# Kernel optimization log

Measured on AMD Instinct MI355X. Metric: run time of the kernel, lower is better.

Reference implementation:

```python
import jax, jax.numpy as jnp
import numpy as np

N_Q_HEADS = 16
N_KV_HEADS = 4
HEAD_DIM = 128
SLIDING_WINDOW = 1024
ROPE_BASE = 1024


def _rope_tables(L, dim):
    # half-truncate RoPE: first dim//4 freqs geometric, next dim//4 zero
    freqs = (1.0 / ROPE_BASE) ** jnp.linspace(0.0, 1.0, num=dim // 4)
    freqs = jnp.concatenate([freqs, jnp.zeros(dim // 4, dtype=freqs.dtype)])
    theta = jnp.arange(L, dtype=jnp.float32)[:, None] * freqs[None, :]  # (L, dim/2)
    cos = jnp.cos(theta)[None, :, None, :]  # (1, L, 1, dim/2)
    sin = jnp.sin(theta)[None, :, None, :]
    return cos, sin


def _rotate(x, cos, sin):
    # x: (B, L, H, D)
    x1, x2 = jnp.split(x, 2, axis=-1)
    return jnp.concatenate([x1 * cos + x2 * sin, -x1 * sin + x2 * cos], axis=-1)


def setup_inputs() -> dict:
    key = jax.random.key(0)
    k1, k2, k3, k4 = jax.random.split(key, 4)
    B, L, D = 1, 2048, 2048
    qkv_dim = (N_Q_HEADS + 2 * N_KV_HEADS) * HEAD_DIM  # 3072
    return {
        "x": jax.random.normal(k1, (B, L, D), dtype=jnp.float32),
        "Wqkv": jax.random.normal(k2, (D, qkv_dim), dtype=jnp.float32) * (D ** -0.5),
        "Wo": jax.random.normal(k3, (N_Q_HEADS * HEAD_DIM, D), dtype=jnp.float32) * ((N_Q_HEADS * HEAD_DIM) ** -0.5),
        "s": jax.random.normal(k4, (1, N_Q_HEADS), dtype=jnp.float32) * 0.1,
    }


def reference(x, Wqkv, Wo, s):
    B, L, D = x.shape
    H, QM, hd = N_KV_HEADS, N_Q_HEADS // N_KV_HEADS, HEAD_DIM

    proj = x @ Wqkv  # (B, L, (Hq + 2*Hkv) * hd)
    q, k, v = jnp.split(proj, (N_Q_HEADS * hd, (N_Q_HEADS + N_KV_HEADS) * hd), axis=-1)

    cos, sin = _rope_tables(L, hd)
    q = _rotate(q.reshape(B, L, -1, hd), cos, sin).reshape(B, L, H, QM, hd)
    k = _rotate(k.reshape(B, L, H, hd), cos, sin)
    v = v.reshape(B, L, H, hd)

    sm_scale = 1.0 / jnp.sqrt(jnp.float32(hd))
    q_pos = jnp.arange(L)[None, :, None]
    k_pos = jnp.arange(L)[None, None, :]
    causal = q_pos >= k_pos                       # (1, L, L)
    window = q_pos < k_pos + SLIDING_WINDOW       # index % 2 == 0 -> window active
    mask = causal & window

    # (B, H, M, Lq, Lk) attention logits
    attn = jnp.einsum("bqhmd,bkhd->bhmqk", q, k) * sm_scale
    # NOTE: faithful to source: -inf placed WHERE mask is True
    attn = jnp.where(mask, -jnp.inf, attn)

    sink = jnp.broadcast_to(s.reshape(B, H, QM, 1, 1), (B, H, QM, L, 1))
    w = jax.nn.softmax(jnp.concatenate([attn, sink], axis=-1), axis=-1)[..., :-1]

    out = jnp.einsum("bhmqk,bkhd->bqhmd", w, v).reshape(B, L, -1)
    return out @ Wo
```

## Files before the change

### kernel.cpp

```cpp
#include <hip/hip_runtime.h>
#include <hip/hip_bf16.h>
#include <math.h>

typedef __bf16 bf16;
typedef __bf16 bf16x8 __attribute__((ext_vector_type(8)));
typedef __bf16 bf16x4v __attribute__((ext_vector_type(4)));
typedef short s16x4 __attribute__((ext_vector_type(4)));
typedef float f32x4 __attribute__((ext_vector_type(4)));

#define GLD16(gp, lp) __builtin_amdgcn_global_load_lds( \
    (__attribute__((address_space(1))) void*)(void*)(gp), \
    (__attribute__((address_space(3))) void*)(lp), 16, 0, 0)

#define L_SEQ 2048
#define D_MODEL 2048
#define QKV_N 3072
#define HD 128
#define QSCALE 0.1275310242959836f
#define LOG2E 1.4426950408889634f

__global__ __launch_bounds__(256) void prep(const float* __restrict__ x,
                                            const float* __restrict__ Wqkv,
                                            const float* __restrict__ Wo,
                                            bf16* __restrict__ xb,
                                            bf16* __restrict__ wqkvT,
                                            bf16* __restrict__ woT) {
    __shared__ float tile[32][33];
    int bid = blockIdx.x;
    if (bid < 4096) {
        int idx = (bid * 256 + threadIdx.x) * 4;
        float4 f = *(const float4*)(x + idx);
        bf16x4v o;
        o.x = (bf16)f.x; o.y = (bf16)f.y; o.z = (bf16)f.z; o.w = (bf16)f.w;
        *(bf16x4v*)(xb + idx) = o;
        return;
    }
    bid -= 4096;
    const float* src; bf16* dst; long ld_s, ld_d; int bx, by;
    if (bid < 6144) { bx = bid % 96; by = bid / 96; src = Wqkv; dst = wqkvT; ld_s = QKV_N; ld_d = D_MODEL; }
    else { bid -= 6144; bx = bid & 63; by = bid >> 6; src = Wo; dst = woT; ld_s = D_MODEL; ld_d = D_MODEL; }
    const int tx = threadIdx.x & 31, ty = threadIdx.x >> 5;
    const long c = bx * 32 + tx, r0 = by * 32;
#pragma unroll
    for (int i = 0; i < 4; ++i)
        tile[ty + i * 8][tx] = src[(r0 + ty + i * 8) * ld_s + c];
    __syncthreads();
    const long c0 = bx * 32;
#pragma unroll
    for (int i = 0; i < 4; ++i)
        dst[(c0 + ty + i * 8) * ld_d + r0 + tx] = (bf16)tile[tx][ty + i * 8];
}

#define GEMM64_BODY(KDIM)                                                        \
    __shared__ __align__(16) bf16 As[64 * 32];                                   \
    __shared__ __align__(16) bf16 Bs[128 * 32];                                  \
    const int tid = threadIdx.x;                                                 \
    const int wid = tid >> 6, lane = tid & 63;                                   \
    const int quad = lane >> 4, l15 = lane & 15;                                 \
    const long m0 = (long)blockIdx.y * 64, n0 = (long)blockIdx.x * 128;          \
    const int srowA = wid * 16 + (lane >> 2);                                    \
    const int srowB = wid * 32 + (lane >> 2);                                    \
    const int scol = ((lane & 3) ^ ((lane >> 3) & 3)) * 8;                       \
    f32x4 acc[8];                                                                \
    _Pragma("unroll")                                                            \
    for (int j = 0; j < 8; ++j) acc[j] = (f32x4){0.f, 0.f, 0.f, 0.f};            \
    const bf16* Ap  = A  + (m0 + srowA) * KDIM + scol;                           \
    const bf16* Bp  = Bt + (n0 + srowB) * KDIM + scol;                           \
    const bf16* Bp2 = Bp + (long)16 * KDIM;                                      \
    bf16* lA  = &As[(wid * 16) * 32];                                            \
    bf16* lB  = &Bs[(wid * 32) * 32];                                            \
    bf16* lB2 = &Bs[(wid * 32 + 16) * 32];                                       \
    const int rsw = ((l15 >> 1) & 3);                                            \
    for (int k0 = 0; k0 < KDIM; k0 += 32) {                                      \
        GLD16(Ap + k0, lA);                                                      \
        GLD16(Bp + k0, lB);                                                      \
        GLD16(Bp2 + k0, lB2);                                                    \
        __syncthreads();                                                         \
        bf16x8 af = *(const bf16x8*)&As[(wid * 16 + l15) * 32 + (quad ^ rsw) * 8]; \
        bf16x8 bfr[8];                                                           \
        _Pragma("unroll")                                                        \
        for (int j = 0; j < 8; ++j)                                              \
            bfr[j] = *(const bf16x8*)&Bs[(j * 16 + l15) * 32 + (quad ^ rsw) * 8]; \
        _Pragma("unroll")                                                        \
        for (int j = 0; j < 8; ++j)                                              \
            acc[j] = __builtin_amdgcn_mfma_f32_16x16x32_bf16(af, bfr[j], acc[j], 0, 0, 0); \
        __syncthreads();                                                         \
    }

__global__ __launch_bounds__(256) void gemm_qkv(const bf16* __restrict__ A,
                                                const bf16* __restrict__ Bt,
                                                bf16* __restrict__ Qb,
                                                bf16* __restrict__ Kb,
                                                bf16* __restrict__ Vtb) {
    const int head = blockIdx.x;
    GEMM64_BODY(D_MODEL)

    if (head < 20) {
        const float sc = head < 16 ? QSCALE : 1.0f;
        bf16* dst = head < 16 ? Qb + (long)head * L_SEQ * HD
                              : Kb + (long)(head - 16) * L_SEQ * HD;
#pragma unroll
        for (int jj = 0; jj < 2; ++jj) {
            const int d0 = jj * 16 + l15;
            const float freq = exp2f((float)d0 * (-10.0f / 31.0f));
#pragma unroll
            for (int r = 0; r < 4; ++r) {
                const long row = m0 + wid * 16 + quad * 4 + r;
                float sn, cs;
                sincosf((float)row * freq, &sn, &cs);
                const float x1 = acc[jj][r], x2 = acc[jj + 4][r];
                dst[row * HD + d0]      = (bf16)((x1 * cs + x2 * sn) * sc);
                dst[row * HD + d0 + 64] = (bf16)((x2 * cs - x1 * sn) * sc);
            }
        }
#pragma unroll
        for (int jj = 2; jj < 4; ++jj) {
            const int d0 = jj * 16 + l15;
#pragma unroll
            for (int r = 0; r < 4; ++r) {
                const long row = m0 + wid * 16 + quad * 4 + r;
                dst[row * HD + d0]      = (bf16)(acc[jj][r] * sc);
                dst[row * HD + d0 + 64] = (bf16)(acc[jj + 4][r] * sc);
            }
        }
    } else {
        bf16* dst = Vtb + (long)(head - 20) * HD * L_SEQ;
        const long m = m0 + wid * 16 + quad * 4;
#pragma unroll
        for (int j = 0; j < 8; ++j) {
            const int d = j * 16 + l15;
            bf16x4v vv;
#pragma unroll
            for (int r = 0; r < 4; ++r) vv[r] = (bf16)acc[j][r];
            *(bf16x4v*)(dst + (long)d * L_SEQ + m) = vv;
        }
    }
}

__global__ __launch_bounds__(256) void gemm_out(const bf16* __restrict__ A,
                                                const bf16* __restrict__ Bt,
                                                float* __restrict__ C) {
    GEMM64_BODY(D_MODEL)
#pragma unroll
    for (int j = 0; j < 8; ++j) {
        const long m = m0 + wid * 16 + quad * 4;
        const long n = n0 + j * 16 + l15;
#pragma unroll
        for (int r = 0; r < 4; ++r)
            C[(m + r) * (long)D_MODEL + n] = acc[j][r];
    }
}

__global__ __launch_bounds__(512, 2) void attn_kernel(const bf16* __restrict__ Qb,
                                                      const bf16* __restrict__ Kb,
                                                      const bf16* __restrict__ Vtb,
                                                      const float* __restrict__ sink,
                                                      bf16* __restrict__ Ob) {
    __shared__ __align__(1024) char smem[131072];

    const int bid = blockIdx.x;
    const int t  = bid & 15;
    const int hq = bid >> 4;
    const int h = hq >> 2;
    const int q0 = t * 128;
    const int tid = threadIdx.x;
    const int wid8 = tid >> 6;
    const int g = wid8 >> 2;
    const int w = wid8 & 3;
    const int lane = tid & 63;
    const int quad = lane >> 4, l15 = lane & 15;

    const bf16* Qg = Qb + (long)hq * L_SEQ * HD;
    const bf16* Kg = Kb + (long)h * L_SEQ * HD;
    const bf16* Vg = Vtb + (long)h * HD * L_SEQ;

    bf16x8 qb[2][4];
#pragma unroll
    for (int rf = 0; rf < 2; ++rf)
#pragma unroll
        for (int kkd = 0; kkd < 4; ++kkd)
            qb[rf][kkd] = *(const bf16x8*)(Qg + (long)(q0 + w * 32 + rf * 16 + l15) * HD
                                              + kkd * 32 + quad * 8);

    f32x4 oaccT[2][8];
#pragma unroll
    for (int rf = 0; rf < 2; ++rf)
#pragma unroll
        for (int j = 0; j < 8; ++j) oaccT[rf][j] = (f32x4){0.f, 0.f, 0.f, 0.f};
    float lacc[2] = {0.f, 0.f};

    const int locnt = (2 * t - 14 > 0) ? (2 * t - 14) : 0;
    const int n = locnt + 32 - 2 * t;
    const int iters = (n + 1) >> 1;

    auto stage = [&](int it2, int buf) {
        const int i = 2 * it2 + g;
        if (i >= n) return;
        const int kt = (i < locnt) ? i : (2 * t + (i - locnt));
        const int k0 = kt * 64;
        bf16* Ksb  = (bf16*)(smem + g * 65536 + buf * 32768);
        bf16* Vtsb = (bf16*)(smem + g * 65536 + buf * 32768 + 16384);
#pragma unroll
        for (int ii = 0; ii < 4; ++ii) {
            int rowb = w * 16 + ii * 4;
            int row = rowb + quad;
            GLD16(Kg + (long)(k0 + row) * HD + ((l15 ^ (row & 7)) * 8), &Ksb[rowb * 128]);
        }
#pragma unroll
        for (int ii = 0; ii < 4; ++ii) {
            int rowb = w * 32 + ii * 8;
            int row = rowb + (lane >> 3);
            GLD16(Vg + (long)row * L_SEQ + k0 + (((lane & 7) ^ (row & 7)) * 8), &Vtsb[rowb * 64]);
        }
    };

    stage(0, 0);

    for (int it = 0; it < iters; ++it) {
        __syncthreads();
        if (it + 1 < iters) stage(it + 1, (it + 1) & 1);

        const int i = 2 * it + g;
        if (i >= n) continue;
        const int kt = (i < locnt) ? i : (2 * t + (i - locnt));
        const int k0 = kt * 64;
        const bf16* Ks  = (const bf16*)(smem + g * 65536 + (it & 1) * 32768);
        const bf16* Vts = (const bf16*)(smem + g * 65536 + (it & 1) * 32768 + 16384);

        f32x4 sacc[2][4];
#pragma unroll
        for (int kb = 0; kb < 4; ++kb) {
            bf16x8 ka[4];
#pragma unroll
            for (int kkd = 0; kkd < 4; ++kkd)
                ka[kkd] = *(const bf16x8*)&Ks[(kb * 16 + l15) * 128 +
                                              (((kkd * 4 + quad) ^ (l15 & 7)) * 8)];
#pragma unroll
            for (int rf = 0; rf < 2; ++rf) {
                f32x4 acc = (f32x4){0.f, 0.f, 0.f, 0.f};
#pragma unroll
                for (int kkd = 0; kkd < 4; ++kkd)
                    acc = __builtin_amdgcn_mfma_f32_16x16x32_bf16(ka[kkd], qb[rf][kkd], acc, 0, 0, 0);
                sacc[rf][kb] = acc;
            }
        }

        const bool bnd = (kt == 2 * t) || (kt == 2 * t + 1) ||
                         (kt == 2 * t - 15) || (kt == 2 * t - 16);
        s16x4 pb[2][4];
#pragma unroll
        for (int rf = 0; rf < 2; ++rf) {
            const int qq = q0 + w * 32 + rf * 16 + l15;
#pragma unroll
            for (int kb = 0; kb < 4; ++kb) {
#pragma unroll
                for (int r = 0; r < 4; ++r) {
                    float v = sacc[rf][kb][r];
                    if (bnd) {
                        const int kk = k0 + kb * 16 + quad * 4 + r;
                        if (!((kk > qq) || (kk <= qq - 1024))) v = -1e30f;
                    }
                    const float p = exp2f(v);
                    lacc[rf] += p;
                    bf16 hp = (bf16)p;
                    pb[rf][kb][r] = __builtin_bit_cast(short, hp);
                }
            }
        }

#pragma unroll
        for (int j = 0; j < 8; ++j) {
            const int drow = j * 16 + l15;
#pragma unroll
            for (int kq = 0; kq < 4; ++kq) {
                const int pc = ((kq * 2 + (quad >> 1)) ^ (l15 & 7));
                s16x4 va = *(const s16x4*)((const char*)&Vts[drow * 64] + pc * 16 + (quad & 1) * 8);
#pragma unroll
                for (int rf = 0; rf < 2; ++rf)
                    oaccT[rf][j] = __builtin_amdgcn_mfma_f32_16x16x16bf16_1k(
                        va, pb[rf][kq], oaccT[rf][j], 0, 0, 0);
            }
        }
    }

#pragma unroll
    for (int rf = 0; rf < 2; ++rf) {
        lacc[rf] += __shfl_xor(lacc[rf], 16, 64);
        lacc[rf] += __shfl_xor(lacc[rf], 32, 64);
    }

    __syncthreads();
    float* Obuf = (float*)smem;
    float* lbuf = (float*)(smem + 67584);
    if (g == 1) {
#pragma unroll
        for (int rf = 0; rf < 2; ++rf) {
            const int ql = w * 32 + rf * 16 + l15;
#pragma unroll
            for (int j = 0; j < 8; ++j)
                *(f32x4*)&Obuf[ql * 132 + j * 16 + quad * 4] = oaccT[rf][j];
            if (quad == 0) lbuf[ql] = lacc[rf];
        }
    }
    __syncthreads();
    if (g == 0) {
        const float sv2 = sink[hq] * LOG2E;
#pragma unroll
        for (int rf = 0; rf < 2; ++rf) {
            const int ql = w * 32 + rf * 16 + l15;
            const float ltot = lacc[rf] + lbuf[ql] + exp2f(sv2);
            const float inv = 1.0f / ltot;
            bf16* dst = Ob + (long)(q0 + ql) * D_MODEL + hq * HD;
#pragma unroll
            for (int j = 0; j < 8; ++j) {
                f32x4 o2 = *(const f32x4*)&Obuf[ql * 132 + j * 16 + quad * 4];
                bf16x4v ov;
#pragma unroll
                for (int r = 0; r < 4; ++r)
                    ov[r] = (bf16)((oaccT[rf][j][r] + o2[r]) * inv);
                *(bf16x4v*)(dst + j * 16 + quad * 4) = ov;
            }
        }
    }
}

extern "C" void kernel_launch(void* const* d_in, const int* in_sizes, int n_in,
                              void* d_out, int out_size, void* d_ws, size_t ws_size,
                              hipStream_t stream) {
    (void)in_sizes; (void)n_in; (void)out_size; (void)ws_size;
    const float* x    = (const float*)d_in[0];
    const float* Wqkv = (const float*)d_in[1];
    const float* Wo   = (const float*)d_in[2];
    const float* s    = (const float*)d_in[3];
    float* out = (float*)d_out;

    char* ws = (char*)d_ws;
    bf16* xb    = (bf16*)ws;  ws += (size_t)D_MODEL * D_MODEL * 2;
    bf16* wqkvT = (bf16*)ws;  ws += (size_t)QKV_N * D_MODEL * 2;
    bf16* woT   = (bf16*)ws;  ws += (size_t)D_MODEL * D_MODEL * 2;
    bf16* Qb    = (bf16*)ws;  ws += (size_t)16 * L_SEQ * HD * 2;
    bf16* Kb    = (bf16*)ws;  ws += (size_t)4 * L_SEQ * HD * 2;
    bf16* Vtb   = (bf16*)ws;  ws += (size_t)4 * HD * L_SEQ * 2;
    bf16* attnb = (bf16*)ws;  ws += (size_t)L_SEQ * D_MODEL * 2;

    prep<<<14336, 256, 0, stream>>>(x, Wqkv, Wo, xb, wqkvT, woT);

    gemm_qkv<<<dim3(QKV_N / 128, L_SEQ / 64), 256, 0, stream>>>(
        xb, wqkvT, Qb, Kb, Vtb);

    attn_kernel<<<256, 512, 0, stream>>>(Qb, Kb, Vtb, s, attnb);

    gemm_out<<<dim3(D_MODEL / 128, L_SEQ / 64), 256, 0, stream>>>(
        attnb, woT, out);
}
```

Before: 232.3 us.

## Split attention key range across separate blocks with a combine kernel

Each 512-thread attention block, whose two wave groups split the key tiles and merged through shared memory, becomes two independent 256-thread blocks. Each new block owns half the key tiles and writes unnormalized bf16 partial outputs and row sums to workspace. A new combine kernel adds the two partials, adds the sink term, normalizes and writes the attention output. The aim is finer-grained scheduling and smaller blocks with less shared memory each. In exchange it adds an extra kernel launch, global traffic for the partials, and bf16 rounding of the partials before they are summed. The workspace is reorganized so the partials reuse the region of the converted input, which is dead after the QKV GEMM.

```diff
diff --git a/kernel.cpp b/kernel.cpp
--- a/kernel.cpp
+++ b/kernel.cpp
@@ -151,22 +151,21 @@
     }
 }
 
-__global__ __launch_bounds__(512, 2) void attn_kernel(const bf16* __restrict__ Qb,
-                                                      const bf16* __restrict__ Kb,
-                                                      const bf16* __restrict__ Vtb,
-                                                      const float* __restrict__ sink,
-                                                      bf16* __restrict__ Ob) {
-    __shared__ __align__(1024) char smem[131072];
+__global__ __launch_bounds__(256, 2) void attn_p(const bf16* __restrict__ Qb,
+                                                 const bf16* __restrict__ Kb,
+                                                 const bf16* __restrict__ Vtb,
+                                                 bf16* __restrict__ Opart,
+                                                 float* __restrict__ lpart) {
+    __shared__ __align__(1024) char smem[65536];
 
     const int bid = blockIdx.x;
-    const int t  = bid & 15;
-    const int hq = bid >> 4;
+    int t, hq, half;
+    if (bid < 256) { t = bid >> 5; hq = (bid & 31) >> 1; half = bid & 1; }
+    else { int b2 = bid - 256; t = 8 + (b2 >> 5); hq = (b2 & 31) >> 1; half = b2 & 1; }
     const int h = hq >> 2;
     const int q0 = t * 128;
     const int tid = threadIdx.x;
-    const int wid8 = tid >> 6;
-    const int g = wid8 >> 2;
-    const int w = wid8 & 3;
+    const int w = tid >> 6;
     const int lane = tid & 63;
     const int quad = lane >> 4, l15 = lane & 15;
 
@@ -191,15 +190,17 @@
 
     const int locnt = (2 * t - 14 > 0) ? (2 * t - 14) : 0;
     const int n = locnt + 32 - 2 * t;
-    const int iters = (n + 1) >> 1;
-
-    auto stage = [&](int it2, int buf) {
-        const int i = 2 * it2 + g;
-        if (i >= n) return;
-        const int kt = (i < locnt) ? i : (2 * t + (i - locnt));
-        const int k0 = kt * 64;
-        bf16* Ksb  = (bf16*)(smem + g * 65536 + buf * 32768);
-        bf16* Vtsb = (bf16*)(smem + g * 65536 + buf * 32768 + 16384);
+    const int cnt = n >> 1;
+
+    auto ktile = [&](int idx) {
+        const int i = 2 * idx + half;
+        return (i < locnt) ? i : (2 * t + (i - locnt));
+    };
+
+    auto stage = [&](int idx, int buf) {
+        const int k0 = ktile(idx) * 64;
+        bf16* Ksb  = (bf16*)(smem + buf * 32768);
+        bf16* Vtsb = (bf16*)(smem + buf * 32768 + 16384);
 #pragma unroll
         for (int ii = 0; ii < 4; ++ii) {
             int rowb = w * 16 + ii * 4;
@@ -216,16 +217,14 @@
 
     stage(0, 0);
 
-    for (int it = 0; it < iters; ++it) {
+    for (int it = 0; it < cnt; ++it) {
         __syncthreads();
-        if (it + 1 < iters) stage(it + 1, (it + 1) & 1);
-
-        const int i = 2 * it + g;
-        if (i >= n) continue;
-        const int kt = (i < locnt) ? i : (2 * t + (i - locnt));
+        if (it + 1 < cnt) stage(it + 1, (it + 1) & 1);
+
+        const int kt = ktile(it);
         const int k0 = kt * 64;
-        const bf16* Ks  = (const bf16*)(smem + g * 65536 + (it & 1) * 32768);
-        const bf16* Vts = (const bf16*)(smem + g * 65536 + (it & 1) * 32768 + 16384);
+        const bf16* Ks  = (const bf16*)(smem + (it & 1) * 32768);
+        const bf16* Vts = (const bf16*)(smem + (it & 1) * 32768 + 16384);
 
         f32x4 sacc[2][4];
 #pragma unroll
@@ -289,39 +288,41 @@
         lacc[rf] += __shfl_xor(lacc[rf], 32, 64);
     }
 
-    __syncthreads();
-    float* Obuf = (float*)smem;
-    float* lbuf = (float*)(smem + 67584);
-    if (g == 1) {
-#pragma unroll
-        for (int rf = 0; rf < 2; ++rf) {
-            const int ql = w * 32 + rf * 16 + l15;
-#pragma unroll
-            for (int j = 0; j < 8; ++j)
-                *(f32x4*)&Obuf[ql * 132 + j * 16 + quad * 4] = oaccT[rf][j];
-            if (quad == 0) lbuf[ql] = lacc[rf];
-        }
-    }
-    __syncthreads();
-    if (g == 0) {
-        const float sv2 = sink[hq] * LOG2E;
-#pragma unroll
-        for (int rf = 0; rf < 2; ++rf) {
-            const int ql = w * 32 + rf * 16 + l15;
-            const float ltot = lacc[rf] + lbuf[ql] + exp2f(sv2);
-            const float inv = 1.0f / ltot;
-            bf16* dst = Ob + (long)(q0 + ql) * D_MODEL + hq * HD;
-#pragma unroll
-            for (int j = 0; j < 8; ++j) {
-                f32x4 o2 = *(const f32x4*)&Obuf[ql * 132 + j * 16 + quad * 4];
-                bf16x4v ov;
-#pragma unroll
-                for (int r = 0; r < 4; ++r)
-                    ov[r] = (bf16)((oaccT[rf][j][r] + o2[r]) * inv);
-                *(bf16x4v*)(dst + j * 16 + quad * 4) = ov;
-            }
-        }
-    }
+    bf16* Od = Opart + (long)bid * 16384;
+#pragma unroll
+    for (int rf = 0; rf < 2; ++rf) {
+        const int ql = w * 32 + rf * 16 + l15;
+#pragma unroll
+        for (int j = 0; j < 8; ++j) {
+            bf16x4v ov;
+#pragma unroll
+            for (int r = 0; r < 4; ++r) ov[r] = (bf16)oaccT[rf][j][r];
+            *(bf16x4v*)(Od + ql * 128 + j * 16 + quad * 4) = ov;
+        }
+        if (quad == 0) lpart[bid * 128 + ql] = lacc[rf];
+    }
+}
+
+__global__ __launch_bounds__(256) void attn_combine(const bf16* __restrict__ Opart,
+                                                    const float* __restrict__ lpart,
+                                                    const float* __restrict__ sink,
+                                                    bf16* __restrict__ attnb) {
+    const int job = blockIdx.x >> 3, sub = blockIdx.x & 7;
+    const int t = job >> 4, hq = job & 15;
+    const int bid0 = (t < 8) ? (t * 32 + hq * 2) : (256 + (t - 8) * 32 + hq * 2);
+    const int bid1 = bid0 + 1;
+    const int e = sub * 2048 + threadIdx.x * 8;
+    const int q = e >> 7, d0 = e & 127;
+    bf16x8 o0 = *(const bf16x8*)(Opart + (long)bid0 * 16384 + q * 128 + d0);
+    bf16x8 o1 = *(const bf16x8*)(Opart + (long)bid1 * 16384 + q * 128 + d0);
+    const float l = lpart[bid0 * 128 + q] + lpart[bid1 * 128 + q] +
+                    exp2f(sink[hq] * LOG2E);
+    const float inv = 1.0f / l;
+    bf16x8 ov;
+#pragma unroll
+    for (int r = 0; r < 8; ++r)
+        ov[r] = (bf16)(((float)o0[r] + (float)o1[r]) * inv);
+    *(bf16x8*)(attnb + (long)(t * 128 + q) * D_MODEL + hq * 128 + d0) = ov;
 }
 
 extern "C" void kernel_launch(void* const* d_in, const int* in_sizes, int n_in,
@@ -335,20 +336,24 @@
     float* out = (float*)d_out;
 
     char* ws = (char*)d_ws;
-    bf16* xb    = (bf16*)ws;  ws += (size_t)D_MODEL * D_MODEL * 2;
-    bf16* wqkvT = (bf16*)ws;  ws += (size_t)QKV_N * D_MODEL * 2;
-    bf16* woT   = (bf16*)ws;  ws += (size_t)D_MODEL * D_MODEL * 2;
-    bf16* Qb    = (bf16*)ws;  ws += (size_t)16 * L_SEQ * HD * 2;
-    bf16* Kb    = (bf16*)ws;  ws += (size_t)4 * L_SEQ * HD * 2;
-    bf16* Vtb   = (bf16*)ws;  ws += (size_t)4 * HD * L_SEQ * 2;
-    bf16* attnb = (bf16*)ws;  ws += (size_t)L_SEQ * D_MODEL * 2;
+    bf16* xb    = (bf16*)ws;
+    bf16* wqkvT = (bf16*)(ws + 8388608);
+    bf16* Qb    = (bf16*)(ws + 20971520);
+    bf16* Kb    = (bf16*)(ws + 29360128);
+    bf16* Vtb   = (bf16*)(ws + 31457280);
+    bf16* woT   = (bf16*)(ws + 33554432);
+    bf16* attnb = (bf16*)(ws + 41943040);
+    bf16* Opart = (bf16*)ws;
+    float* lpart = (float*)(ws + 16777216);
 
     prep<<<14336, 256, 0, stream>>>(x, Wqkv, Wo, xb, wqkvT, woT);
 
     gemm_qkv<<<dim3(QKV_N / 128, L_SEQ / 64), 256, 0, stream>>>(
         xb, wqkvT, Qb, Kb, Vtb);
 
-    attn_kernel<<<256, 512, 0, stream>>>(Qb, Kb, Vtb, s, attnb);
+    attn_p<<<512, 256, 0, stream>>>(Qb, Kb, Vtb, Opart, lpart);
+
+    attn_combine<<<2048, 256, 0, stream>>>(Opart, lpart, s, attnb);
 
     gemm_out<<<dim3(D_MODEL / 128, L_SEQ / 64), 256, 0, stream>>>(
         attnb, woT, out);
```

Result: faster. 224.7 us (-3.3%).
